# Performance work log

Measured on AMD Instinct MI355X. Metric: run time of the kernel, lower is better.

Reference implementation:

```python
import jax, jax.numpy as jnp
import numpy as np

N_EMBD, D_INNER, DT_RANK, D_CONV, D_STATE, SEQ_LEN = 2048, 4096, 128, 4, 16, 2048


def setup_inputs() -> dict:
    key = jax.random.key(0)
    ks = jax.random.split(key, 8)
    sc = lambda fan_in: 1.0 / np.sqrt(fan_in)
    x = jax.random.normal(ks[0], (SEQ_LEN, N_EMBD), dtype=jnp.float32)
    in_proj_w = jax.random.normal(ks[1], (2 * D_INNER, N_EMBD), jnp.float32) * sc(N_EMBD)
    in_proj_b = jnp.zeros((2 * D_INNER,), jnp.float32)
    conv_w = jax.random.normal(ks[2], (D_INNER, 1, D_CONV), jnp.float32) * sc(D_CONV)
    conv_b = jnp.zeros((D_INNER,), jnp.float32)
    ssm_in_w = jax.random.normal(ks[3], (DT_RANK + 2 * D_STATE, D_INNER), jnp.float32) * sc(D_INNER)
    delta_w = jax.random.normal(ks[4], (D_INNER, DT_RANK), jnp.float32) * sc(DT_RANK)
    # A_log init exactly as module: repeat(arange(1,d_state+1), d_inner).reshape(d_inner,d_state)
    A_log = jnp.log(jnp.repeat(jnp.arange(1, D_STATE + 1), D_INNER).reshape(D_INNER, D_STATE).astype(jnp.float32))
    D = jnp.ones((D_INNER,), jnp.float32)
    out_w = jax.random.normal(ks[5], (N_EMBD, D_INNER), jnp.float32) * sc(D_INNER)
    out_b = jnp.zeros((N_EMBD,), jnp.float32)
    return {"x": x, "in_proj_w": in_proj_w, "in_proj_b": in_proj_b, "conv_w": conv_w,
            "conv_b": conv_b, "ssm_in_w": ssm_in_w, "delta_w": delta_w, "A_log": A_log,
            "D": D, "out_w": out_w, "out_b": out_b}


def selective_scan(u, delta, A, B, C, D):
    # u, delta: (L, di); A: (di, ds); B, C: (L, ds); D: (di,)
    dA = jnp.exp(delta[:, :, None] * A[None, :, :])                # (L, di, ds)
    dBu = delta[:, :, None] * B[:, None, :] * u[:, :, None]        # (L, di, ds)

    def step(h, inp):
        dA_t, dBu_t, C_t = inp
        h = dA_t * h + dBu_t                                       # (di, ds)
        y = jnp.einsum('ds,s->d', h, C_t)
        return h, y

    h0 = jnp.zeros((u.shape[1], A.shape[1]), u.dtype)
    _, ys = jax.lax.scan(step, h0, (dA, dBu, C))
    return ys + u * D                                              # (L, di)


def mamba_block(x, in_proj_w, in_proj_b, conv_w, conv_b, ssm_in_w, delta_w, A_log, D, out_w, out_b):
    L = x.shape[0]
    xr = x @ in_proj_w.T + in_proj_b                               # (L, 2*di)
    xi, res = jnp.split(xr, 2, axis=-1)
    # depthwise causal conv1d: left-pad d_conv-1 (== first L outputs of symmetric pad)
    xc = jax.lax.conv_general_dilated(
        xi.T[None],                                                # (1, di, L)
        conv_w,                                                    # (di, 1, k)
        window_strides=(1,), padding=[(D_CONV - 1, 0)],
        feature_group_count=D_INNER)[0] + conv_b[:, None]
    xc = jax.nn.silu(xc.T)                                         # (L, di)
    # SSM
    A = -jnp.exp(A_log)
    dbc = xc @ ssm_in_w.T                                          # (L, dt_rank + 2*ds)
    delta, B, C = jnp.split(dbc, [DT_RANK, DT_RANK + D_STATE], axis=-1)
    delta = jax.nn.softplus(delta @ delta_w.T)                     # (L, di)
    y = selective_scan(xc, delta, A, B, C, D)
    y = y * jax.nn.silu(res)
    return y @ out_w.T + out_b                                     # (L, n_embd)


def reference(x, in_proj_w, in_proj_b, conv_w, conv_b, ssm_in_w, delta_w, A_log, D, out_w, out_b):
    return mamba_block(x, in_proj_w, in_proj_b, conv_w, conv_b, ssm_in_w, delta_w, A_log, D, out_w, out_b)
```

## Files before the change

### kernel.cpp

```cpp
#include <hip/hip_runtime.h>
#include <cstdint>
#include <cstddef>


typedef __bf16 bf16x8 __attribute__((ext_vector_type(8)));
typedef float f32x4 __attribute__((ext_vector_type(4)));

#define GLDS16(g, l)                                        \
  __builtin_amdgcn_global_load_lds(                         \
      (__attribute__((address_space(1))) void*)(g),         \
      (__attribute__((address_space(3))) void*)(l), 16, 0, 0)

#define FENCE() asm volatile("" ::: "memory")
#define BARRIER()                      \
  do {                                 \
    FENCE();                           \
    __builtin_amdgcn_s_barrier();      \
    FENCE();                           \
  } while (0)

static __device__ __forceinline__ unsigned short f2b(float f) {
  unsigned int x = __builtin_bit_cast(unsigned int, f);
  x += 0x7fffu + ((x >> 16) & 1u);
  return (unsigned short)(x >> 16);
}

static __device__ __forceinline__ float b2f(unsigned short u) {
  return __builtin_bit_cast(float, (unsigned int)u << 16);
}

static __device__ __forceinline__ float sigmoidf_fast(float x) {
  return 1.0f / (1.0f + __expf(-x));
}

struct CastArgs {
  const float* src[5];
  unsigned short* dst[5];
  int n4[5];
};

__global__ __launch_bounds__(256) void cast_multi(CastArgs a) {
  const int stride = gridDim.x * 256;
  const int t = blockIdx.x * 256 + threadIdx.x;
#pragma unroll
  for (int k = 0; k < 5; ++k) {
    const float4* src = reinterpret_cast<const float4*>(a.src[k]);
    ushort4* dst = reinterpret_cast<ushort4*>(a.dst[k]);
    const int n4 = a.n4[k];
    for (int i = t; i < n4; i += stride) {
      float4 v = src[i];
      ushort4 o;
      o.x = f2b(v.x); o.y = f2b(v.y); o.z = f2b(v.z); o.w = f2b(v.w);
      dst[i] = o;
    }
  }
}

template <int MODE>
__global__ __launch_bounds__(512) void gemm256_bt(
    const unsigned short* __restrict__ A, const unsigned short* __restrict__ B,
    float* __restrict__ Cp, unsigned short* __restrict__ xib,
    unsigned short* __restrict__ rsb, const float* __restrict__ bias,
    int M, int N, int K, int Kslice) {
  __shared__ __align__(16) unsigned short lds[65536];
  const int tid = threadIdx.x;
  const int l = tid & 63;
  const int w = tid >> 6;
  const int wr = w >> 2;
  const int wc = w & 3;

  const int nwg = gridDim.x * gridDim.y;
  const int q = nwg >> 3;
  int flat = blockIdx.x + gridDim.x * blockIdx.y;
  flat = (flat & 7) * q + (flat >> 3);
  const int bx = flat % gridDim.x;
  const int by = flat / gridDim.x;

  const long brow = (long)bx * 256;
  const long bcol = (long)by * 256;
  const int ks = blockIdx.z;
  const int NT = Kslice >> 6;

  f32x4 acc[8][4] = {};

  const unsigned short* Ab = A + (size_t)brow * K + (size_t)ks * Kslice;
  const unsigned short* Bb = B + (size_t)bcol * K + (size_t)ks * Kslice;
  size_t soff[4];
  int doff[4];
#pragma unroll
  for (int i = 0; i < 4; ++i) {
    int idx = i * 512 + tid;
    int r = idx >> 3, s = idx & 7;
    soff[i] = (size_t)r * K + (size_t)((s ^ (r & 7)) << 3);
    doff[i] = idx * 8;
  }

  auto stage = [&](int kt, int buf) {
    const int k0 = kt << 6;
#pragma unroll
    for (int i = 0; i < 4; ++i)
      GLDS16(Ab + soff[i] + k0, &lds[buf * 32768 + doff[i]]);
#pragma unroll
    for (int i = 0; i < 4; ++i)
      GLDS16(Bb + soff[i] + k0, &lds[buf * 32768 + 16384 + doff[i]]);
  };

  const int hi = l >> 4, lo7 = l & 7;
  const int sw0 = ((0 + hi) ^ lo7) << 3;
  const int sw1 = ((4 + hi) ^ lo7) << 3;
  const int rowA = wr * 128 + (l & 15);
  const int colB = wc * 64 + (l & 15);

  stage(0, 0);
  stage(1, 1);

  int buf = 0;
  for (int kt = 0; kt < NT; ++kt) {
    const bool last = (kt == NT - 1);
    if (last) {
      asm volatile("s_waitcnt vmcnt(0)" ::: "memory");
    } else {
      asm volatile("s_waitcnt vmcnt(8)" ::: "memory");
    }
    BARRIER();
    const int bb = buf * 32768;
    bf16x8 a0[8], b0[4];
#pragma unroll
    for (int m = 0; m < 8; ++m)
      a0[m] = *reinterpret_cast<const bf16x8*>(&lds[bb + (rowA + m * 16) * 64 + sw0]);
#pragma unroll
    for (int n = 0; n < 4; ++n)
      b0[n] = *reinterpret_cast<const bf16x8*>(&lds[bb + 16384 + (colB + n * 16) * 64 + sw0]);
    __builtin_amdgcn_s_setprio(1);
#pragma unroll
    for (int m = 0; m < 8; ++m)
#pragma unroll
      for (int n = 0; n < 4; ++n)
        acc[m][n] = __builtin_amdgcn_mfma_f32_16x16x32_bf16(a0[m], b0[n], acc[m][n], 0, 0, 0);
    __builtin_amdgcn_s_setprio(0);
    bf16x8 a1[8], b1[4];
#pragma unroll
    for (int m = 0; m < 8; ++m)
      a1[m] = *reinterpret_cast<const bf16x8*>(&lds[bb + (rowA + m * 16) * 64 + sw1]);
#pragma unroll
    for (int n = 0; n < 4; ++n)
      b1[n] = *reinterpret_cast<const bf16x8*>(&lds[bb + 16384 + (colB + n * 16) * 64 + sw1]);
    asm volatile("s_waitcnt lgkmcnt(0)" ::: "memory");
    __builtin_amdgcn_sched_barrier(0);
    BARRIER();
    if (kt + 2 < NT) stage(kt + 2, buf);
    __builtin_amdgcn_s_setprio(1);
#pragma unroll
    for (int m = 0; m < 8; ++m)
#pragma unroll
      for (int n = 0; n < 4; ++n)
        acc[m][n] = __builtin_amdgcn_mfma_f32_16x16x32_bf16(a1[m], b1[n], acc[m][n], 0, 0, 0);
    __builtin_amdgcn_s_setprio(0);
    buf ^= 1;
  }

  const long r0 = brow + wr * 128 + (l >> 4) * 4;
  const long c0 = bcol + wc * 64 + (l & 15);
  if (MODE == 1) {
    float* Cb = Cp + (size_t)ks * M * N;
#pragma unroll
    for (int m = 0; m < 8; ++m)
#pragma unroll
      for (int n = 0; n < 4; ++n) {
        long col = c0 + n * 16;
#pragma unroll
        for (int r = 0; r < 4; ++r)
          Cb[(r0 + m * 16 + r) * (long)N + col] = acc[m][n][r];
      }
  } else {
#pragma unroll
    for (int m = 0; m < 8; ++m)
#pragma unroll
      for (int n = 0; n < 4; ++n) {
        long col = c0 + n * 16;
        float bv = bias[col];
        const bool isres = col >= 4096;
        long cc = isres ? col - 4096 : col;
#pragma unroll
        for (int r = 0; r < 4; ++r) {
          float v = acc[m][n][r] + bv;
          if (isres) {
            float s = v * sigmoidf_fast(v);
            rsb[(r0 + m * 16 + r) * 4096 + cc] = f2b(s);
          } else {
            xib[(r0 + m * 16 + r) * 4096 + cc] = f2b(v);
          }
        }
      }
  }
}

__global__ __launch_bounds__(256) void reduce4_bias(
    const float* __restrict__ part, const float* __restrict__ bias,
    float* __restrict__ out, int n4) {
  int stride = gridDim.x * 256;
  for (int f = blockIdx.x * 256 + threadIdx.x; f < n4; f += stride) {
    float4 s0 = reinterpret_cast<const float4*>(part)[f];
    float4 s1 = reinterpret_cast<const float4*>(part + 4194304ull)[f];
    float4 s2 = reinterpret_cast<const float4*>(part + 8388608ull)[f];
    float4 s3 = reinterpret_cast<const float4*>(part + 12582912ull)[f];
    float4 bv = reinterpret_cast<const float4*>(bias)[f & 511];
    float4 o;
    o.x = s0.x + s1.x + s2.x + s3.x + bv.x;
    o.y = s0.y + s1.y + s2.y + s3.y + bv.y;
    o.z = s0.z + s1.z + s2.z + s3.z + bv.z;
    o.w = s0.w + s1.w + s2.w + s3.w + bv.w;
    reinterpret_cast<float4*>(out)[f] = o;
  }
}

__global__ __launch_bounds__(256) void gemm_bt_sp(
    const unsigned short* __restrict__ A, const unsigned short* __restrict__ B,
    float* __restrict__ C, int M, int N, int K) {
  __shared__ __align__(16) unsigned short lA[128 * 32];
  __shared__ __align__(16) unsigned short lB[128 * 32];
  const int tid = threadIdx.x;
  const int l = tid & 63;
  const int w = tid >> 6;
  const int wr = w >> 1, wc = w & 1;
  const long brow = (long)blockIdx.x * 128;
  const long bcol = (long)blockIdx.y * 128;

  f32x4 acc[4][4] = {};

  const int srow = tid >> 2;
  const int scol = (tid & 3) * 8;

  const unsigned short* Ab = A + (size_t)brow * K;
  const unsigned short* Bb = B + (size_t)bcol * K;

  for (int k0 = 0; k0 < K; k0 += 32) {
#pragma unroll
    for (int j = 0; j < 2; ++j) {
      GLDS16(Ab + (size_t)(j * 64 + srow) * K + k0 + scol, &lA[j * 2048 + tid * 8]);
      GLDS16(Bb + (size_t)(j * 64 + srow) * K + k0 + scol, &lB[j * 2048 + tid * 8]);
    }
    __syncthreads();
    bf16x8 af[4], bfr[4];
#pragma unroll
    for (int mt = 0; mt < 4; ++mt)
      af[mt] = *reinterpret_cast<const bf16x8*>(
          &lA[(wr * 64 + mt * 16 + (l & 15)) * 32 + (l >> 4) * 8]);
#pragma unroll
    for (int nt = 0; nt < 4; ++nt)
      bfr[nt] = *reinterpret_cast<const bf16x8*>(
          &lB[(wc * 64 + nt * 16 + (l & 15)) * 32 + (l >> 4) * 8]);
#pragma unroll
    for (int mt = 0; mt < 4; ++mt)
#pragma unroll
      for (int nt = 0; nt < 4; ++nt)
        acc[mt][nt] = __builtin_amdgcn_mfma_f32_16x16x32_bf16(
            af[mt], bfr[nt], acc[mt][nt], 0, 0, 0);
    __syncthreads();
  }

  const long r0 = brow + wr * 64 + ((l >> 4) * 4);
  const long c0 = bcol + wc * 64 + (l & 15);
#pragma unroll
  for (int mt = 0; mt < 4; ++mt) {
#pragma unroll
    for (int nt = 0; nt < 4; ++nt) {
      long col = c0 + nt * 16;
#pragma unroll
      for (int r = 0; r < 4; ++r) {
        long row = r0 + mt * 16 + r;
        float v = acc[mt][nt][r];
        v = (v > 20.0f) ? v : log1pf(__expf(v));
        C[row * (long)N + col] = v;
      }
    }
  }
}

__global__ __launch_bounds__(256) void conv_silu_k(
    const unsigned short* __restrict__ xib, const float* __restrict__ cw,
    const float* __restrict__ cb, unsigned short* __restrict__ xcb) {
  const int d = blockIdx.x * 256 + threadIdx.x;
  const int t0 = blockIdx.y * 128;
  const float4 wv = *reinterpret_cast<const float4*>(cw + (size_t)d * 4);
  const float bv = cb[d];
  float xm3 = (t0 >= 3) ? b2f(xib[(size_t)(t0 - 3) * 4096 + d]) : 0.0f;
  float xm2 = (t0 >= 2) ? b2f(xib[(size_t)(t0 - 2) * 4096 + d]) : 0.0f;
  float xm1 = (t0 >= 1) ? b2f(xib[(size_t)(t0 - 1) * 4096 + d]) : 0.0f;
  for (int tt = 0; tt < 128; ++tt) {
    const size_t t = (size_t)t0 + tt;
    float xt = b2f(xib[t * 4096 + d]);
    float a = bv + wv.x * xm3 + wv.y * xm2 + wv.z * xm1 + wv.w * xt;
    float s = a * sigmoidf_fast(a);
    xcb[t * 4096 + d] = f2b(s);
    xm3 = xm2; xm2 = xm1; xm1 = xt;
  }
}

__global__ __launch_bounds__(256) void gemm_dbc(
    const unsigned short* __restrict__ A, const unsigned short* __restrict__ B,
    float* __restrict__ part) {
  __shared__ __align__(16) unsigned short lA[64 * 32];
  __shared__ __align__(16) unsigned short lB[160 * 32];
  const int tid = threadIdx.x;
  const int l = tid & 63, w = tid >> 6;
  const int brow = blockIdx.x * 64;
  const int ks = blockIdx.y;
  const int K = 4096;
  f32x4 acc[10] = {};
  const int srow = tid >> 2, scol = (tid & 3) * 8;
  for (int k0 = ks * 512; k0 < ks * 512 + 512; k0 += 32) {
    GLDS16(A + (size_t)(brow + srow) * K + k0 + scol, &lA[tid * 8]);
#pragma unroll
    for (int j = 0; j < 3; ++j) {
      int li = j * 256 + tid;
      if (li < 640) {
        GLDS16(B + (size_t)(li >> 2) * K + k0 + (li & 3) * 8, &lB[li * 8]);
      }
    }
    __syncthreads();
    bf16x8 af = *reinterpret_cast<const bf16x8*>(
        &lA[(w * 16 + (l & 15)) * 32 + (l >> 4) * 8]);
#pragma unroll
    for (int nt = 0; nt < 10; ++nt) {
      bf16x8 bfr = *reinterpret_cast<const bf16x8*>(
          &lB[(nt * 16 + (l & 15)) * 32 + (l >> 4) * 8]);
      acc[nt] = __builtin_amdgcn_mfma_f32_16x16x32_bf16(af, bfr, acc[nt], 0, 0, 0);
    }
    __syncthreads();
  }
  const int r0 = brow + w * 16 + (l >> 4) * 4;
  const int c = l & 15;
#pragma unroll
  for (int nt = 0; nt < 10; ++nt)
#pragma unroll
    for (int r = 0; r < 4; ++r)
      part[((size_t)ks * 2048 + r0 + r) * 160 + nt * 16 + c] = acc[nt][r];
}

__global__ __launch_bounds__(256) void reduce_dbc(
    const float* __restrict__ part, unsigned short* __restrict__ drb,
    float* __restrict__ bc) {
  int idx = blockIdx.x * 256 + threadIdx.x;
  float s = 0.0f;
#pragma unroll
  for (int k = 0; k < 8; ++k) s += part[(size_t)k * 2048 * 160 + idx];
  int row = idx / 160, col = idx - row * 160;
  if (col < 128) drb[row * 128 + col] = f2b(s);
  else bc[row * 32 + (col - 128)] = s;
}

__global__ __launch_bounds__(256) void scan_passA(
    const float* __restrict__ delta, const unsigned short* __restrict__ xcb,
    const float* __restrict__ bc, const float* __restrict__ alog,
    float* __restrict__ P, float* __restrict__ S) {
  __shared__ float lbc[1024];
  const int d = blockIdx.x * 256 + threadIdx.x;
  const int c = blockIdx.y;
  const int t0 = c * 32;
#pragma unroll
  for (int j = 0; j < 4; ++j) {
    int idx = j * 256 + threadIdx.x;
    lbc[idx] = bc[(size_t)t0 * 32 + idx];
  }
  __syncthreads();
  float a[16], h[16], p[16];
#pragma unroll
  for (int s = 0; s < 16; ++s) {
    a[s] = -__expf(alog[(size_t)d * 16 + s]);
    h[s] = 0.0f;
    p[s] = 1.0f;
  }
  for (int tt = 0; tt < 32; ++tt) {
    float dt = delta[(size_t)(t0 + tt) * 4096 + d];
    float u = b2f(xcb[(size_t)(t0 + tt) * 4096 + d]);
    float du = dt * u;
#pragma unroll
    for (int s = 0; s < 16; ++s) {
      float e = __expf(dt * a[s]);
      h[s] = e * h[s] + du * lbc[tt * 32 + s];
      p[s] *= e;
    }
  }
  size_t o = ((size_t)c * 4096 + d) * 16;
#pragma unroll
  for (int s = 0; s < 16; s += 4) {
    *reinterpret_cast<float4*>(&P[o + s]) = make_float4(p[s], p[s + 1], p[s + 2], p[s + 3]);
    *reinterpret_cast<float4*>(&S[o + s]) = make_float4(h[s], h[s + 1], h[s + 2], h[s + 3]);
  }
}

__global__ __launch_bounds__(256) void scan_passB(
    float* __restrict__ P, const float* __restrict__ S) {
  const int idx = blockIdx.x * 256 + threadIdx.x;
  float h = 0.0f;
  for (int c = 0; c < 64; ++c) {
    size_t o = (size_t)c * 65536 + idx;
    float p = P[o], sv = S[o];
    P[o] = h;
    h = p * h + sv;
  }
}

__global__ __launch_bounds__(256) void scan_passC(
    const float* __restrict__ delta, const unsigned short* __restrict__ xcb,
    const float* __restrict__ bc, const float* __restrict__ alog,
    const float* __restrict__ hst, const float* __restrict__ Dp,
    const unsigned short* __restrict__ rsb, unsigned short* __restrict__ yb) {
  __shared__ float lbc[1024];
  const int d = blockIdx.x * 256 + threadIdx.x;
  const int c = blockIdx.y;
  const int t0 = c * 32;
#pragma unroll
  for (int j = 0; j < 4; ++j) {
    int idx = j * 256 + threadIdx.x;
    lbc[idx] = bc[(size_t)t0 * 32 + idx];
  }
  __syncthreads();
  float a[16], h[16];
  size_t o = ((size_t)c * 4096 + d) * 16;
#pragma unroll
  for (int s = 0; s < 16; ++s) {
    a[s] = -__expf(alog[(size_t)d * 16 + s]);
    h[s] = hst[o + s];
  }
  const float Dv = Dp[d];
  for (int tt = 0; tt < 32; ++tt) {
    float dt = delta[(size_t)(t0 + tt) * 4096 + d];
    float u = b2f(xcb[(size_t)(t0 + tt) * 4096 + d]);
    float du = dt * u;
    float y = 0.0f;
#pragma unroll
    for (int s = 0; s < 16; ++s) {
      float e = __expf(dt * a[s]);
      h[s] = e * h[s] + du * lbc[tt * 32 + s];
      y += h[s] * lbc[tt * 32 + 16 + s];
    }
    float rs = b2f(rsb[(size_t)(t0 + tt) * 4096 + d]);
    float v = (y + u * Dv) * rs;
    yb[(size_t)(t0 + tt) * 4096 + d] = f2b(v);
  }
}

extern "C" void kernel_launch(void* const* d_in, const int* in_sizes, int n_in,
                              void* d_out, int out_size, void* d_ws, size_t ws_size,
                              hipStream_t stream) {
  const float* x    = (const float*)d_in[0];
  const float* w1   = (const float*)d_in[1];
  const float* b1   = (const float*)d_in[2];
  const float* cw   = (const float*)d_in[3];
  const float* cb   = (const float*)d_in[4];
  const float* w2   = (const float*)d_in[5];
  const float* w3   = (const float*)d_in[6];
  const float* alog = (const float*)d_in[7];
  const float* Dp   = (const float*)d_in[8];
  const float* w4   = (const float*)d_in[9];
  const float* b4   = (const float*)d_in[10];
  float* out = (float*)d_out;

  char* ws = (char*)d_ws;
  size_t off = 0;
  auto alloc = [&](size_t b) {
    size_t o = off;
    off += (b + 255) & ~(size_t)255;
    return o;
  };
  unsigned short* w1b = (unsigned short*)(ws + alloc(2ull * 8192 * 2048));
  unsigned short* xb  = (unsigned short*)(ws + alloc(2ull * 2048 * 2048));
  unsigned short* w2b = (unsigned short*)(ws + alloc(2ull * 160 * 4096));
  unsigned short* w3b = (unsigned short*)(ws + alloc(2ull * 4096 * 128));
  unsigned short* w4b = (unsigned short*)(ws + alloc(2ull * 2048 * 4096));
  unsigned short* xib = (unsigned short*)(ws + alloc(2ull * 2048 * 4096));
  unsigned short* rsb = (unsigned short*)(ws + alloc(2ull * 2048 * 4096));
  unsigned short* xcb = (unsigned short*)(ws + alloc(2ull * 2048 * 4096));
  unsigned short* drb = (unsigned short*)(ws + alloc(2ull * 2048 * 128));
  float* bcb  = (float*)(ws + alloc(4ull * 2048 * 32));
  float* delta = (float*)(ws + alloc(4ull * 2048 * 4096));
  float* P = (float*)(ws + alloc(4ull * 64 * 4096 * 16));
  float* S = (float*)(ws + alloc(4ull * 64 * 4096 * 16));
  float* part  = delta;
  unsigned short* yb = xib;
  float* part4 = delta;

  if (ws_size < off) return;

  CastArgs ca;
  ca.src[0] = w1; ca.dst[0] = w1b; ca.n4[0] = 8192 * 2048 / 4;
  ca.src[1] = x;  ca.dst[1] = xb;  ca.n4[1] = 2048 * 2048 / 4;
  ca.src[2] = w2; ca.dst[2] = w2b; ca.n4[2] = 160 * 4096 / 4;
  ca.src[3] = w3; ca.dst[3] = w3b; ca.n4[3] = 4096 * 128 / 4;
  ca.src[4] = w4; ca.dst[4] = w4b; ca.n4[4] = 2048 * 4096 / 4;
  cast_multi<<<2048, 256, 0, stream>>>(ca);

  gemm256_bt<2><<<dim3(8, 32, 1), 512, 0, stream>>>(
      xb, w1b, nullptr, xib, rsb, b1, 2048, 8192, 2048, 2048);
  conv_silu_k<<<dim3(16, 16), 256, 0, stream>>>(xib, cw, cb, xcb);
  gemm_dbc<<<dim3(32, 8), 256, 0, stream>>>(xcb, w2b, part);
  reduce_dbc<<<1280, 256, 0, stream>>>(part, drb, bcb);
  gemm_bt_sp<<<dim3(16, 32), 256, 0, stream>>>(drb, w3b, delta, 2048, 4096, 128);
  scan_passA<<<dim3(16, 64), 256, 0, stream>>>(delta, xcb, bcb, alog, P, S);
  scan_passB<<<256, 256, 0, stream>>>(P, S);
  scan_passC<<<dim3(16, 64), 256, 0, stream>>>(delta, xcb, bcb, alog, P, Dp, rsb, yb);
  gemm256_bt<1><<<dim3(8, 8, 4), 512, 0, stream>>>(
      yb, w4b, part4, nullptr, nullptr, nullptr, 2048, 2048, 4096, 1024);
  reduce4_bias<<<1024, 256, 0, stream>>>(part4, b4, out, 2048 * 2048 / 4);
}
```

Measured before the change: 315.2 us.

## Retile GEMMs with triple-buffered LDS, drop split-K, and lengthen scan chunks

The input-projection GEMM moves from 256x256 to 256x128 tiles with a three-stage LDS ring, giving 512 workgroups instead of 256. The output GEMM drops split-K and the separate reduction kernel in favour of a 128x128-tile kernel that adds the bias and writes the result directly. The scan chunk length doubles from 32 to 64 timesteps, halving the chunk count, the P/S buffers and the serial pass-B loop. Together these aim to improve CU occupancy and remove the partial-sum round trip, at the cost of less parallelism in the scan passes and more LDS reloading per output in the smaller tiles.

```diff
diff --git a/kernel.cpp b/kernel.cpp
--- a/kernel.cpp
+++ b/kernel.cpp
@@ -56,18 +56,16 @@
   }
 }
 
-template <int MODE>
-__global__ __launch_bounds__(512) void gemm256_bt(
+__global__ __launch_bounds__(512) void gemmG1(
     const unsigned short* __restrict__ A, const unsigned short* __restrict__ B,
-    float* __restrict__ Cp, unsigned short* __restrict__ xib,
-    unsigned short* __restrict__ rsb, const float* __restrict__ bias,
-    int M, int N, int K, int Kslice) {
-  __shared__ __align__(16) unsigned short lds[65536];
+    unsigned short* __restrict__ xib, unsigned short* __restrict__ rsb,
+    const float* __restrict__ bias, int M, int N, int K) {
+  __shared__ __align__(16) unsigned short lds[73728];
   const int tid = threadIdx.x;
   const int l = tid & 63;
   const int w = tid >> 6;
-  const int wr = w >> 2;
-  const int wc = w & 3;
+  const int wr = w >> 1;
+  const int wc = w & 1;
 
   const int nwg = gridDim.x * gridDim.y;
   const int q = nwg >> 3;
@@ -77,140 +75,197 @@
   const int by = flat / gridDim.x;
 
   const long brow = (long)bx * 256;
-  const long bcol = (long)by * 256;
-  const int ks = blockIdx.z;
-  const int NT = Kslice >> 6;
-
-  f32x4 acc[8][4] = {};
-
-  const unsigned short* Ab = A + (size_t)brow * K + (size_t)ks * Kslice;
-  const unsigned short* Bb = B + (size_t)bcol * K + (size_t)ks * Kslice;
-  size_t soff[4];
-  int doff[4];
+  const long bcol = (long)by * 128;
+  const int NT = K >> 6;
+
+  f32x4 acc[4][4] = {};
+
+  const unsigned short* Ab = A + (size_t)brow * K;
+  const unsigned short* Bb = B + (size_t)bcol * K;
+
+  size_t soffA[4], soffB[2];
+  int doffA[4], doffB[2];
 #pragma unroll
   for (int i = 0; i < 4; ++i) {
+    int idx = i * 512 + tid;
+    int r = idx >> 3, s = idx & 7;
+    soffA[i] = (size_t)r * K + (size_t)((s ^ (r & 7)) << 3);
+    doffA[i] = idx * 8;
+  }
+#pragma unroll
+  for (int i = 0; i < 2; ++i) {
+    int idx = i * 512 + tid;
+    int r = idx >> 3, s = idx & 7;
+    soffB[i] = (size_t)r * K + (size_t)((s ^ (r & 7)) << 3);
+    doffB[i] = idx * 8;
+  }
+
+  auto stage = [&](int kt) {
+    const int bb = (kt % 3) * 24576;
+    const int k0 = kt << 6;
+#pragma unroll
+    for (int i = 0; i < 4; ++i) GLDS16(Ab + soffA[i] + k0, &lds[bb + doffA[i]]);
+#pragma unroll
+    for (int i = 0; i < 2; ++i) GLDS16(Bb + soffB[i] + k0, &lds[bb + 16384 + doffB[i]]);
+  };
+
+  const int la = l & 15, hi = l >> 4, lo7 = l & 7;
+  const int sw0 = (hi ^ lo7) << 3;
+  const int sw1 = ((hi + 4) ^ lo7) << 3;
+  const int rowA = wr * 64 + la;
+  const int colB = wc * 64 + la;
+
+  stage(0);
+  stage(1);
+
+  for (int kt = 0; kt < NT; ++kt) {
+    if (kt + 1 < NT) asm volatile("s_waitcnt vmcnt(6)" ::: "memory");
+    else             asm volatile("s_waitcnt vmcnt(0)" ::: "memory");
+    BARRIER();
+    const int bb = (kt % 3) * 24576;
+    bf16x8 af[4][2], bf[4][2];
+#pragma unroll
+    for (int mt = 0; mt < 4; ++mt) {
+      af[mt][0] = *reinterpret_cast<const bf16x8*>(&lds[bb + (rowA + mt * 16) * 64 + sw0]);
+      af[mt][1] = *reinterpret_cast<const bf16x8*>(&lds[bb + (rowA + mt * 16) * 64 + sw1]);
+    }
+#pragma unroll
+    for (int nt = 0; nt < 4; ++nt) {
+      bf[nt][0] = *reinterpret_cast<const bf16x8*>(&lds[bb + 16384 + (colB + nt * 16) * 64 + sw0]);
+      bf[nt][1] = *reinterpret_cast<const bf16x8*>(&lds[bb + 16384 + (colB + nt * 16) * 64 + sw1]);
+    }
+    if (kt + 2 < NT) stage(kt + 2);
+    __builtin_amdgcn_s_setprio(1);
+#pragma unroll
+    for (int kk = 0; kk < 2; ++kk)
+#pragma unroll
+      for (int mt = 0; mt < 4; ++mt)
+#pragma unroll
+        for (int nt = 0; nt < 4; ++nt)
+          acc[mt][nt] = __builtin_amdgcn_mfma_f32_16x16x32_bf16(
+              af[mt][kk], bf[nt][kk], acc[mt][nt], 0, 0, 0);
+    __builtin_amdgcn_s_setprio(0);
+  }
+
+  const long r0 = brow + wr * 64 + (l >> 4) * 4;
+  const long c0 = bcol + wc * 64 + (l & 15);
+#pragma unroll
+  for (int mt = 0; mt < 4; ++mt) {
+#pragma unroll
+    for (int nt = 0; nt < 4; ++nt) {
+      const long col = c0 + nt * 16;
+      const float bv = bias[col];
+      const bool isres = col >= 4096;
+      const long cc = isres ? col - 4096 : col;
+#pragma unroll
+      for (int r = 0; r < 4; ++r) {
+        float v = acc[mt][nt][r] + bv;
+        if (isres) {
+          float s = v * sigmoidf_fast(v);
+          rsb[(r0 + mt * 16 + r) * 4096 + cc] = f2b(s);
+        } else {
+          xib[(r0 + mt * 16 + r) * 4096 + cc] = f2b(v);
+        }
+      }
+    }
+  }
+}
+
+__global__ __launch_bounds__(512) void gemm128_bt(
+    const unsigned short* __restrict__ A, const unsigned short* __restrict__ B,
+    float* __restrict__ C, const float* __restrict__ bias,
+    int M, int N, int K) {
+  __shared__ __align__(16) unsigned short lds[49152];
+  const int tid = threadIdx.x;
+  const int l = tid & 63;
+  const int w = tid >> 6;
+  const int wr = w >> 2;
+  const int wc = w & 3;
+
+  const int nwg = gridDim.x * gridDim.y;
+  const int q = nwg >> 3;
+  int flat = blockIdx.x + gridDim.x * blockIdx.y;
+  flat = (flat & 7) * q + (flat >> 3);
+  const int bx = flat % gridDim.x;
+  const int by = flat / gridDim.x;
+
+  const long brow = (long)bx * 128;
+  const long bcol = (long)by * 128;
+  const int NT = K >> 6;
+
+  f32x4 acc[4][2] = {};
+
+  const unsigned short* Ab = A + (size_t)brow * K;
+  const unsigned short* Bb = B + (size_t)bcol * K;
+  size_t soff[2];
+  int doff[2];
+#pragma unroll
+  for (int i = 0; i < 2; ++i) {
     int idx = i * 512 + tid;
     int r = idx >> 3, s = idx & 7;
     soff[i] = (size_t)r * K + (size_t)((s ^ (r & 7)) << 3);
     doff[i] = idx * 8;
   }
 
-  auto stage = [&](int kt, int buf) {
+  auto stage = [&](int kt) {
+    const int bb = (kt % 3) * 16384;
     const int k0 = kt << 6;
 #pragma unroll
-    for (int i = 0; i < 4; ++i)
-      GLDS16(Ab + soff[i] + k0, &lds[buf * 32768 + doff[i]]);
-#pragma unroll
-    for (int i = 0; i < 4; ++i)
-      GLDS16(Bb + soff[i] + k0, &lds[buf * 32768 + 16384 + doff[i]]);
+    for (int i = 0; i < 2; ++i) GLDS16(Ab + soff[i] + k0, &lds[bb + doff[i]]);
+#pragma unroll
+    for (int i = 0; i < 2; ++i) GLDS16(Bb + soff[i] + k0, &lds[bb + 8192 + doff[i]]);
   };
 
-  const int hi = l >> 4, lo7 = l & 7;
-  const int sw0 = ((0 + hi) ^ lo7) << 3;
-  const int sw1 = ((4 + hi) ^ lo7) << 3;
-  const int rowA = wr * 128 + (l & 15);
-  const int colB = wc * 64 + (l & 15);
-
-  stage(0, 0);
-  stage(1, 1);
-
-  int buf = 0;
+  const int la = l & 15, hi = l >> 4, lo7 = l & 7;
+  const int sw0 = (hi ^ lo7) << 3;
+  const int sw1 = ((hi + 4) ^ lo7) << 3;
+  const int rowA = wr * 64 + la;
+  const int colB = wc * 32 + la;
+
+  stage(0);
+  stage(1);
+
   for (int kt = 0; kt < NT; ++kt) {
-    const bool last = (kt == NT - 1);
-    if (last) {
-      asm volatile("s_waitcnt vmcnt(0)" ::: "memory");
-    } else {
-      asm volatile("s_waitcnt vmcnt(8)" ::: "memory");
-    }
+    if (kt + 1 < NT) asm volatile("s_waitcnt vmcnt(4)" ::: "memory");
+    else             asm volatile("s_waitcnt vmcnt(0)" ::: "memory");
     BARRIER();
-    const int bb = buf * 32768;
-    bf16x8 a0[8], b0[4];
-#pragma unroll
-    for (int m = 0; m < 8; ++m)
-      a0[m] = *reinterpret_cast<const bf16x8*>(&lds[bb + (rowA + m * 16) * 64 + sw0]);
-#pragma unroll
-    for (int n = 0; n < 4; ++n)
-      b0[n] = *reinterpret_cast<const bf16x8*>(&lds[bb + 16384 + (colB + n * 16) * 64 + sw0]);
+    const int bb = (kt % 3) * 16384;
+    bf16x8 af[4][2], bf[2][2];
+#pragma unroll
+    for (int mt = 0; mt < 4; ++mt) {
+      af[mt][0] = *reinterpret_cast<const bf16x8*>(&lds[bb + (rowA + mt * 16) * 64 + sw0]);
+      af[mt][1] = *reinterpret_cast<const bf16x8*>(&lds[bb + (rowA + mt * 16) * 64 + sw1]);
+    }
+#pragma unroll
+    for (int nt = 0; nt < 2; ++nt) {
+      bf[nt][0] = *reinterpret_cast<const bf16x8*>(&lds[bb + 8192 + (colB + nt * 16) * 64 + sw0]);
+      bf[nt][1] = *reinterpret_cast<const bf16x8*>(&lds[bb + 8192 + (colB + nt * 16) * 64 + sw1]);
+    }
+    if (kt + 2 < NT) stage(kt + 2);
     __builtin_amdgcn_s_setprio(1);
 #pragma unroll
-    for (int m = 0; m < 8; ++m)
-#pragma unroll
-      for (int n = 0; n < 4; ++n)
-        acc[m][n] = __builtin_amdgcn_mfma_f32_16x16x32_bf16(a0[m], b0[n], acc[m][n], 0, 0, 0);
+    for (int kk = 0; kk < 2; ++kk)
+#pragma unroll
+      for (int mt = 0; mt < 4; ++mt)
+#pragma unroll
+        for (int nt = 0; nt < 2; ++nt)
+          acc[mt][nt] = __builtin_amdgcn_mfma_f32_16x16x32_bf16(
+              af[mt][kk], bf[nt][kk], acc[mt][nt], 0, 0, 0);
     __builtin_amdgcn_s_setprio(0);
-    bf16x8 a1[8], b1[4];
-#pragma unroll
-    for (int m = 0; m < 8; ++m)
-      a1[m] = *reinterpret_cast<const bf16x8*>(&lds[bb + (rowA + m * 16) * 64 + sw1]);
-#pragma unroll
-    for (int n = 0; n < 4; ++n)
-      b1[n] = *reinterpret_cast<const bf16x8*>(&lds[bb + 16384 + (colB + n * 16) * 64 + sw1]);
-    asm volatile("s_waitcnt lgkmcnt(0)" ::: "memory");
-    __builtin_amdgcn_sched_barrier(0);
-    BARRIER();
-    if (kt + 2 < NT) stage(kt + 2, buf);
-    __builtin_amdgcn_s_setprio(1);
-#pragma unroll
-    for (int m = 0; m < 8; ++m)
-#pragma unroll
-      for (int n = 0; n < 4; ++n)
-        acc[m][n] = __builtin_amdgcn_mfma_f32_16x16x32_bf16(a1[m], b1[n], acc[m][n], 0, 0, 0);
-    __builtin_amdgcn_s_setprio(0);
-    buf ^= 1;
-  }
-
-  const long r0 = brow + wr * 128 + (l >> 4) * 4;
-  const long c0 = bcol + wc * 64 + (l & 15);
-  if (MODE == 1) {
-    float* Cb = Cp + (size_t)ks * M * N;
-#pragma unroll
-    for (int m = 0; m < 8; ++m)
-#pragma unroll
-      for (int n = 0; n < 4; ++n) {
-        long col = c0 + n * 16;
-#pragma unroll
-        for (int r = 0; r < 4; ++r)
-          Cb[(r0 + m * 16 + r) * (long)N + col] = acc[m][n][r];
-      }
-  } else {
-#pragma unroll
-    for (int m = 0; m < 8; ++m)
-#pragma unroll
-      for (int n = 0; n < 4; ++n) {
-        long col = c0 + n * 16;
-        float bv = bias[col];
-        const bool isres = col >= 4096;
-        long cc = isres ? col - 4096 : col;
-#pragma unroll
-        for (int r = 0; r < 4; ++r) {
-          float v = acc[m][n][r] + bv;
-          if (isres) {
-            float s = v * sigmoidf_fast(v);
-            rsb[(r0 + m * 16 + r) * 4096 + cc] = f2b(s);
-          } else {
-            xib[(r0 + m * 16 + r) * 4096 + cc] = f2b(v);
-          }
-        }
-      }
-  }
-}
-
-__global__ __launch_bounds__(256) void reduce4_bias(
-    const float* __restrict__ part, const float* __restrict__ bias,
-    float* __restrict__ out, int n4) {
-  int stride = gridDim.x * 256;
-  for (int f = blockIdx.x * 256 + threadIdx.x; f < n4; f += stride) {
-    float4 s0 = reinterpret_cast<const float4*>(part)[f];
-    float4 s1 = reinterpret_cast<const float4*>(part + 4194304ull)[f];
-    float4 s2 = reinterpret_cast<const float4*>(part + 8388608ull)[f];
-    float4 s3 = reinterpret_cast<const float4*>(part + 12582912ull)[f];
-    float4 bv = reinterpret_cast<const float4*>(bias)[f & 511];
-    float4 o;
-    o.x = s0.x + s1.x + s2.x + s3.x + bv.x;
-    o.y = s0.y + s1.y + s2.y + s3.y + bv.y;
-    o.z = s0.z + s1.z + s2.z + s3.z + bv.z;
-    o.w = s0.w + s1.w + s2.w + s3.w + bv.w;
-    reinterpret_cast<float4*>(out)[f] = o;
+  }
+
+  const long r0 = brow + wr * 64 + (l >> 4) * 4;
+  const long c0 = bcol + wc * 32 + (l & 15);
+#pragma unroll
+  for (int mt = 0; mt < 4; ++mt) {
+#pragma unroll
+    for (int nt = 0; nt < 2; ++nt) {
+      long col = c0 + nt * 16;
+      float bv = bias[col];
+#pragma unroll
+      for (int r = 0; r < 4; ++r)
+        C[(r0 + mt * 16 + r) * (long)N + col] = acc[mt][nt][r] + bv;
+    }
   }
 }
 
@@ -354,12 +409,12 @@
     const float* __restrict__ delta, const unsigned short* __restrict__ xcb,
     const float* __restrict__ bc, const float* __restrict__ alog,
     float* __restrict__ P, float* __restrict__ S) {
-  __shared__ float lbc[1024];
+  __shared__ float lbc[2048];
   const int d = blockIdx.x * 256 + threadIdx.x;
   const int c = blockIdx.y;
-  const int t0 = c * 32;
-#pragma unroll
-  for (int j = 0; j < 4; ++j) {
+  const int t0 = c * 64;
+#pragma unroll
+  for (int j = 0; j < 8; ++j) {
     int idx = j * 256 + threadIdx.x;
     lbc[idx] = bc[(size_t)t0 * 32 + idx];
   }
@@ -371,7 +426,7 @@
     h[s] = 0.0f;
     p[s] = 1.0f;
   }
-  for (int tt = 0; tt < 32; ++tt) {
+  for (int tt = 0; tt < 64; ++tt) {
     float dt = delta[(size_t)(t0 + tt) * 4096 + d];
     float u = b2f(xcb[(size_t)(t0 + tt) * 4096 + d]);
     float du = dt * u;
@@ -394,7 +449,7 @@
     float* __restrict__ P, const float* __restrict__ S) {
   const int idx = blockIdx.x * 256 + threadIdx.x;
   float h = 0.0f;
-  for (int c = 0; c < 64; ++c) {
+  for (int c = 0; c < 32; ++c) {
     size_t o = (size_t)c * 65536 + idx;
     float p = P[o], sv = S[o];
     P[o] = h;
@@ -407,12 +462,12 @@
     const float* __restrict__ bc, const float* __restrict__ alog,
     const float* __restrict__ hst, const float* __restrict__ Dp,
     const unsigned short* __restrict__ rsb, unsigned short* __restrict__ yb) {
-  __shared__ float lbc[1024];
+  __shared__ float lbc[2048];
   const int d = blockIdx.x * 256 + threadIdx.x;
   const int c = blockIdx.y;
-  const int t0 = c * 32;
-#pragma unroll
-  for (int j = 0; j < 4; ++j) {
+  const int t0 = c * 64;
+#pragma unroll
+  for (int j = 0; j < 8; ++j) {
     int idx = j * 256 + threadIdx.x;
     lbc[idx] = bc[(size_t)t0 * 32 + idx];
   }
@@ -425,7 +480,7 @@
     h[s] = hst[o + s];
   }
   const float Dv = Dp[d];
-  for (int tt = 0; tt < 32; ++tt) {
+  for (int tt = 0; tt < 64; ++tt) {
     float dt = delta[(size_t)(t0 + tt) * 4096 + d];
     float u = b2f(xcb[(size_t)(t0 + tt) * 4096 + d]);
     float du = dt * u;
@@ -476,11 +531,10 @@
   unsigned short* drb = (unsigned short*)(ws + alloc(2ull * 2048 * 128));
   float* bcb  = (float*)(ws + alloc(4ull * 2048 * 32));
   float* delta = (float*)(ws + alloc(4ull * 2048 * 4096));
-  float* P = (float*)(ws + alloc(4ull * 64 * 4096 * 16));
-  float* S = (float*)(ws + alloc(4ull * 64 * 4096 * 16));
+  float* P = (float*)(ws + alloc(4ull * 32 * 4096 * 16));
+  float* S = (float*)(ws + alloc(4ull * 32 * 4096 * 16));
   float* part  = delta;
   unsigned short* yb = xib;
-  float* part4 = delta;
 
   if (ws_size < off) return;
 
@@ -492,16 +546,14 @@
   ca.src[4] = w4; ca.dst[4] = w4b; ca.n4[4] = 2048 * 4096 / 4;
   cast_multi<<<2048, 256, 0, stream>>>(ca);
 
-  gemm256_bt<2><<<dim3(8, 32, 1), 512, 0, stream>>>(
-      xb, w1b, nullptr, xib, rsb, b1, 2048, 8192, 2048, 2048);
+  gemmG1<<<dim3(8, 64), 512, 0, stream>>>(
+      xb, w1b, xib, rsb, b1, 2048, 8192, 2048);
   conv_silu_k<<<dim3(16, 16), 256, 0, stream>>>(xib, cw, cb, xcb);
   gemm_dbc<<<dim3(32, 8), 256, 0, stream>>>(xcb, w2b, part);
   reduce_dbc<<<1280, 256, 0, stream>>>(part, drb, bcb);
   gemm_bt_sp<<<dim3(16, 32), 256, 0, stream>>>(drb, w3b, delta, 2048, 4096, 128);
-  scan_passA<<<dim3(16, 64), 256, 0, stream>>>(delta, xcb, bcb, alog, P, S);
+  scan_passA<<<dim3(16, 32), 256, 0, stream>>>(delta, xcb, bcb, alog, P, S);
   scan_passB<<<256, 256, 0, stream>>>(P, S);
-  scan_passC<<<dim3(16, 64), 256, 0, stream>>>(delta, xcb, bcb, alog, P, Dp, rsb, yb);
-  gemm256_bt<1><<<dim3(8, 8, 4), 512, 0, stream>>>(
-      yb, w4b, part4, nullptr, nullptr, nullptr, 2048, 2048, 4096, 1024);
-  reduce4_bias<<<1024, 256, 0, stream>>>(part4, b4, out, 2048 * 2048 / 4);
-}
+  scan_passC<<<dim3(16, 32), 256, 0, stream>>>(delta, xcb, bcb, alog, P, Dp, rsb, yb);
+  gemm128_bt<<<dim3(16, 16), 512, 0, stream>>>(yb, w4b, out, b4, 2048, 2048, 4096);
+}
```

Result: slower. 322.1 us (+2.2%).
